# Performance work log

Hardware: AMD Instinct MI355X
Metric: run time of the kernel (lower is better)

Reference implementation:

```python
import jax, jax.numpy as jnp
import numpy as np

NUM_LAYERS = 2      # args.num_layers
EPS = 1e-6          # poincare_to_lorentz eps
NORM_CLIP = 1.0     # exp_map norm_control clip
N, K, F, D = 30000, 32, 256, 128


def _normalize_lorentz(h):
    # project onto hyperboloid: time = sqrt(1 + |space|^2)
    sp = h[:, 1:]
    t = jnp.sqrt(1.0 + jnp.sum(sp * sp, axis=-1, keepdims=True))
    return jnp.concatenate([t, sp], axis=-1)


def _exp_map_zero(v):
    # tangent vector at origin has zero time component (normalize_tan with x=0)
    sp = v[:, 1:]
    ldv = jnp.sum(sp * sp, axis=-1, keepdims=True)          # Lorentz norm^2 of (0, sp)
    nd = jnp.sqrt(jnp.clip(ldv + 1e-9, 1e-10, None))
    t = jnp.minimum(nd, NORM_CLIP)                           # norm_control
    time = jnp.cosh(t)
    space = jnp.sinh(t) * sp / nd
    return _normalize_lorentz(jnp.concatenate([time, space], axis=-1))


def _hyperbolic_mean(nbr, w):
    # nbr: [N, K, D] Lorentz points; w: [N, K] neighbor weights
    k = nbr[..., 1:] / nbr[..., :1]                          # h2k: Klein model
    kn = jnp.clip(jnp.sum(k * k, axis=-1, keepdims=True), 0.0, 0.9)
    lam = w[..., None] / jnp.sqrt(1.0 - kn)                  # weighted Lorentz factors
    k_mean = jnp.sum(lam * k, axis=1) / jnp.sum(lam, axis=1)  # [N, D-1]
    # k2h: Klein -> hyperboloid
    kn2 = jnp.minimum(jnp.sum(k_mean * k_mean, axis=-1, keepdims=True), 0.9)
    ones = jnp.ones((k_mean.shape[0], 1), k_mean.dtype)
    return jnp.concatenate([ones, k_mean], axis=-1) / jnp.sqrt(1.0 - kn2)


def _lorentz_activation(h):
    # lorentz -> poincare, SELU, poincare -> lorentz (c = 1)
    p = h[:, 1:] / (h[:, :1] + 1.0)
    p = jax.nn.selu(p)
    pn = jnp.sum(p * p, axis=-1, keepdims=True)
    return jnp.concatenate([1.0 + pn, 2.0 * p], axis=-1) / (1.0 - pn + EPS)


def setup_inputs() -> dict:
    key = jax.random.key(0)
    k1, k2, k3, k4, k5 = jax.random.split(key, 5)
    x = jax.random.normal(k1, (N, F), dtype=jnp.float32)
    adj = jax.random.randint(k2, (N, K), 0, N, dtype=jnp.int32)
    w = jax.random.uniform(k3, (N, K), dtype=jnp.float32)
    lin_W = jax.random.normal(k4, (F, D), dtype=jnp.float32) / np.sqrt(F)
    lin_b = jnp.zeros((D,), dtype=jnp.float32)
    M, _ = jnp.linalg.qr(jax.random.normal(k5, (D - 1, D - 1), dtype=jnp.float32))  # orthogonal init
    return {"x": x, "adj": adj, "w": w, "lin_W": lin_W, "lin_b": lin_b, "M": M}


def reference(x, adj, w, lin_W, lin_b, M):
    h = jax.nn.selu(x @ lin_W + lin_b)          # Euclidean projection + activation
    h = _exp_map_zero(h)                        # lift to hyperboloid
    d = h.shape[-1]
    # retrieve_params: block-diag [[1,0],[0,M]] Lorentz rotation (tie_weight -> shared)
    lw = jnp.zeros((d, d), h.dtype).at[0, 0].set(1.0).at[1:, 1:].set(M)
    for _ in range(NUM_LAYERS):
        msg = h @ lw                             # Stiefel transform
        nbr = msg[adj]                           # [N, K, D] neighbor gather
        h = _hyperbolic_mean(nbr, w)             # Klein weighted mean
        h = _lorentz_activation(h)               # SELU in Poincare model
        h = _normalize_lorentz(h)                # re-project onto hyperboloid
    return h
```

## Files before the change

### kernel.cpp

```cpp
#include <hip/hip_runtime.h>
#include <hip/hip_fp16.h>
#include <math.h>

#define NN 30000
#define KK 32
#define FF 256
#define DD 128
#define NB16 1875
#define SA 268

typedef _Float16 f16x8 __attribute__((ext_vector_type(8)));
typedef float f32x4v __attribute__((ext_vector_type(4)));

__device__ __forceinline__ float seluf(float x) {
    const float scale = 1.0507009873554804934193349852946f;
    const float alpha = 1.6732632423543772848170429916717f;
    return x > 0.f ? scale * x : scale * alpha * expm1f(x);
}

__device__ __forceinline__ float waveReduceSum(float v) {
#pragma unroll
    for (int m = 1; m < 64; m <<= 1) v += __shfl_xor(v, m, 64);
    return v;
}

__global__ __launch_bounds__(256) void k_prep(
    const float* __restrict__ W, const float* __restrict__ M,
    _Float16* __restrict__ Wt, _Float16* __restrict__ Lt)
{
    const int b = blockIdx.x, t = threadIdx.x;
    if (b < 128) {
        Wt[b * FF + t] = (_Float16)W[t * DD + b];
    } else if (t < 128) {
        const int c = b - 128, k = t;
        const float v = (k == 0 && c == 0) ? 1.f
                      : ((k >= 1 && c >= 1) ? M[(k - 1) * 127 + (c - 1)] : 0.f);
        Lt[c * DD + k] = (_Float16)v;
    }
}

__global__ __launch_bounds__(256) void k_lin_exp_msg(
    const float* __restrict__ x, const _Float16* __restrict__ Wt,
    const float* __restrict__ b, const _Float16* __restrict__ Lt,
    __half* __restrict__ table)
{
    __shared__ _Float16 as_[16][SA];
    __shared__ _Float16 hhi[16][SA];
    __shared__ _Float16 hlo[16][SA];
    __shared__ float red[4][16];
    __shared__ float m0s[16];
    const int wv_ = threadIdx.x >> 6;
    const int lane = threadIdx.x & 63;
    const int g = lane >> 4, c16 = lane & 15;
    const int baseRow = blockIdx.x * 16;
    const int nb = wv_ * 2;
    const int arow = baseRow + c16;

    {
        const float4* xp = (const float4*)(x + (size_t)arow * FF);
#pragma unroll
        for (int i = 0; i < 2; ++i) {
            const int ks = wv_ * 2 + i;
            const float4 f0 = xp[ks * 8 + g * 2];
            const float4 f1 = xp[ks * 8 + g * 2 + 1];
            const float q[8] = {f0.x, f0.y, f0.z, f0.w, f1.x, f1.y, f1.z, f1.w};
            f16x8 a;
#pragma unroll
            for (int j = 0; j < 8; ++j) a[j] = (_Float16)q[j];
            *(f16x8*)&as_[c16][ks * 32 + g * 8] = a;
        }
    }
    __syncthreads();

    f16x8 bw0[8], bw1[8];
#pragma unroll
    for (int ks = 0; ks < 8; ++ks) {
        bw0[ks] = *(const f16x8*)(Wt + (size_t)((nb + 0) * 16 + c16) * FF + ks * 32 + g * 8);
        bw1[ks] = *(const f16x8*)(Wt + (size_t)((nb + 1) * 16 + c16) * FF + ks * 32 + g * 8);
    }
    f16x8 af[8];
#pragma unroll
    for (int ks = 0; ks < 8; ++ks)
        af[ks] = *(const f16x8*)&as_[c16][ks * 32 + g * 8];

    f32x4v acc[2];
    acc[0] = acc[1] = f32x4v{0.f, 0.f, 0.f, 0.f};
#pragma unroll
    for (int ks = 0; ks < 8; ++ks) {
        acc[0] = __builtin_amdgcn_mfma_f32_16x16x32_f16(af[ks], bw0[ks], acc[0], 0, 0, 0);
        acc[1] = __builtin_amdgcn_mfma_f32_16x16x32_f16(af[ks], bw1[ks], acc[1], 0, 0, 0);
    }

    float bias[2];
#pragma unroll
    for (int n = 0; n < 2; ++n) bias[n] = b[(nb + n) * 16 + c16];

    float vv[4][2];
#pragma unroll
    for (int r = 0; r < 4; ++r) {
        float part = 0.f;
#pragma unroll
        for (int n = 0; n < 2; ++n) {
            vv[r][n] = seluf(acc[n][r] + bias[n]);
            float sq = vv[r][n] * vv[r][n];
            if (wv_ == 0 && n == 0 && c16 == 0) sq = 0.f;
            part += sq;
        }
#pragma unroll
        for (int m = 1; m < 16; m <<= 1) part += __shfl_xor(part, m, 64);
        if (c16 == 0) red[wv_][4 * g + r] = part;
    }
    __syncthreads();
#pragma unroll
    for (int r = 0; r < 4; ++r) {
        const int lrow = 4 * g + r;
        const float ldv = red[0][lrow] + red[1][lrow] + red[2][lrow] + red[3][lrow];
        const float nd = sqrtf(fmaxf(ldv + 1e-9f, 1e-10f));
        const float t  = fminf(nd, 1.0f);
        const float sc = sinhf(t) / nd;
        const float tm = sqrtf(1.f + sc * sc * ldv);
#pragma unroll
        for (int n = 0; n < 2; ++n) {
            const int col = (nb + n) * 16 + c16;
            const float o = (wv_ == 0 && n == 0 && c16 == 0) ? tm : sc * vv[r][n];
            const _Float16 hi = (_Float16)o;
            hhi[lrow][col] = hi;
            hlo[lrow][col] = (_Float16)(o - (float)hi);
        }
    }
    __syncthreads();

    f16x8 bl0[4], bl1[4];
#pragma unroll
    for (int ks = 0; ks < 4; ++ks) {
        bl0[ks] = *(const f16x8*)(Lt + (size_t)((nb + 0) * 16 + c16) * DD + ks * 32 + g * 8);
        bl1[ks] = *(const f16x8*)(Lt + (size_t)((nb + 1) * 16 + c16) * DD + ks * 32 + g * 8);
    }
    f16x8 mh[4], ml[4];
#pragma unroll
    for (int ks = 0; ks < 4; ++ks) {
        mh[ks] = *(const f16x8*)&hhi[c16][ks * 32 + g * 8];
        ml[ks] = *(const f16x8*)&hlo[c16][ks * 32 + g * 8];
    }
    acc[0] = acc[1] = f32x4v{0.f, 0.f, 0.f, 0.f};
#pragma unroll
    for (int ks = 0; ks < 4; ++ks) {
        acc[0] = __builtin_amdgcn_mfma_f32_16x16x32_f16(mh[ks], bl0[ks], acc[0], 0, 0, 0);
        acc[0] = __builtin_amdgcn_mfma_f32_16x16x32_f16(ml[ks], bl0[ks], acc[0], 0, 0, 0);
        acc[1] = __builtin_amdgcn_mfma_f32_16x16x32_f16(mh[ks], bl1[ks], acc[1], 0, 0, 0);
        acc[1] = __builtin_amdgcn_mfma_f32_16x16x32_f16(ml[ks], bl1[ks], acc[1], 0, 0, 0);
    }

#pragma unroll
    for (int r = 0; r < 4; ++r) {
        float part = 0.f;
#pragma unroll
        for (int n = 0; n < 2; ++n) {
            float sq = acc[n][r] * acc[n][r];
            if (wv_ == 0 && n == 0 && c16 == 0) sq = 0.f;
            part += sq;
        }
#pragma unroll
        for (int m = 1; m < 16; m <<= 1) part += __shfl_xor(part, m, 64);
        if (c16 == 0) red[wv_][4 * g + r] = part;
        if (wv_ == 0 && c16 == 0) m0s[4 * g + r] = acc[0][r];
    }
    __syncthreads();
#pragma unroll
    for (int r = 0; r < 4; ++r) {
        const int lrow = 4 * g + r;
        const int row = baseRow + lrow;
        const float rn = 1.f / m0s[lrow];
        const float sum2 = red[0][lrow] + red[1][lrow] + red[2][lrow] + red[3][lrow];
        float kn = sum2 * rn * rn;
        kn = fminf(fmaxf(kn, 0.f), 0.9f);
        const float fh = 1.f / sqrtf(1.f - kn);
#pragma unroll
        for (int n = 0; n < 2; ++n) {
            const float val = (wv_ == 0 && n == 0 && c16 == 0) ? fh : acc[n][r] * rn;
            table[(size_t)row * DD + (nb + n) * 16 + c16] = __float2half(val);
        }
    }
}

__global__ __launch_bounds__(256) void k_msg_aux(
    const float* __restrict__ h, const _Float16* __restrict__ Lt,
    __half* __restrict__ table)
{
    __shared__ _Float16 hhi[16][SA];
    __shared__ _Float16 hlo[16][SA];
    __shared__ float red[4][16];
    __shared__ float m0s[16];
    const int wv_ = threadIdx.x >> 6;
    const int lane = threadIdx.x & 63;
    const int g = lane >> 4, c16 = lane & 15;
    const int baseRow = blockIdx.x * 16;
    const int nb = wv_ * 2;
    const int arow = baseRow + c16;

    {
        const float4* hp = (const float4*)(h + (size_t)arow * DD);
        const int ks = wv_;
        const float4 f0 = hp[ks * 8 + g * 2];
        const float4 f1 = hp[ks * 8 + g * 2 + 1];
        const float q[8] = {f0.x, f0.y, f0.z, f0.w, f1.x, f1.y, f1.z, f1.w};
        f16x8 hi, lo;
#pragma unroll
        for (int j = 0; j < 8; ++j) {
            hi[j] = (_Float16)q[j];
            lo[j] = (_Float16)(q[j] - (float)hi[j]);
        }
        *(f16x8*)&hhi[c16][ks * 32 + g * 8] = hi;
        *(f16x8*)&hlo[c16][ks * 32 + g * 8] = lo;
    }
    __syncthreads();

    f16x8 bl0[4], bl1[4];
#pragma unroll
    for (int ks = 0; ks < 4; ++ks) {
        bl0[ks] = *(const f16x8*)(Lt + (size_t)((nb + 0) * 16 + c16) * DD + ks * 32 + g * 8);
        bl1[ks] = *(const f16x8*)(Lt + (size_t)((nb + 1) * 16 + c16) * DD + ks * 32 + g * 8);
    }
    f16x8 mh[4], ml[4];
#pragma unroll
    for (int ks = 0; ks < 4; ++ks) {
        mh[ks] = *(const f16x8*)&hhi[c16][ks * 32 + g * 8];
        ml[ks] = *(const f16x8*)&hlo[c16][ks * 32 + g * 8];
    }
    f32x4v acc[2];
    acc[0] = acc[1] = f32x4v{0.f, 0.f, 0.f, 0.f};
#pragma unroll
    for (int ks = 0; ks < 4; ++ks) {
        acc[0] = __builtin_amdgcn_mfma_f32_16x16x32_f16(mh[ks], bl0[ks], acc[0], 0, 0, 0);
        acc[0] = __builtin_amdgcn_mfma_f32_16x16x32_f16(ml[ks], bl0[ks], acc[0], 0, 0, 0);
        acc[1] = __builtin_amdgcn_mfma_f32_16x16x32_f16(mh[ks], bl1[ks], acc[1], 0, 0, 0);
        acc[1] = __builtin_amdgcn_mfma_f32_16x16x32_f16(ml[ks], bl1[ks], acc[1], 0, 0, 0);
    }

#pragma unroll
    for (int r = 0; r < 4; ++r) {
        float part = 0.f;
#pragma unroll
        for (int n = 0; n < 2; ++n) {
            float sq = acc[n][r] * acc[n][r];
            if (wv_ == 0 && n == 0 && c16 == 0) sq = 0.f;
            part += sq;
        }
#pragma unroll
        for (int m = 1; m < 16; m <<= 1) part += __shfl_xor(part, m, 64);
        if (c16 == 0) red[wv_][4 * g + r] = part;
        if (wv_ == 0 && c16 == 0) m0s[4 * g + r] = acc[0][r];
    }
    __syncthreads();
#pragma unroll
    for (int r = 0; r < 4; ++r) {
        const int lrow = 4 * g + r;
        const int row = baseRow + lrow;
        const float rn = 1.f / m0s[lrow];
        const float sum2 = red[0][lrow] + red[1][lrow] + red[2][lrow] + red[3][lrow];
        float kn = sum2 * rn * rn;
        kn = fminf(fmaxf(kn, 0.f), 0.9f);
        const float fh = 1.f / sqrtf(1.f - kn);
#pragma unroll
        for (int n = 0; n < 2; ++n) {
            const float val = (wv_ == 0 && n == 0 && c16 == 0) ? fh : acc[n][r] * rn;
            table[(size_t)row * DD + (nb + n) * 16 + c16] = __float2half(val);
        }
    }
}

__global__ __launch_bounds__(256) void k_layer(
    const __half* __restrict__ table, const int* __restrict__ adj,
    const float* __restrict__ w, float* __restrict__ out)
{
    const int wave = threadIdx.x >> 6;
    const int lane = threadIdx.x & 63;
    const int node = blockIdx.x * 4 + wave;

    const int   av = adj[node * KK + (lane & 31)];
    const float wv = w[node * KK + (lane & 31)];

    unsigned int vbits[32];
#pragma unroll
    for (int j = 0; j < KK; ++j) {
        const int idx = __shfl(av, j, 64);
        vbits[j] = *(const unsigned int*)(table + (size_t)idx * DD + lane * 2);
    }

    const float f  = __half2float(table[(size_t)av * DD]);
    const float lam = wv * f;
    float ls = lam;
#pragma unroll
    for (int m = 1; m < 32; m <<= 1) ls += __shfl_xor(ls, m, 64);

    float km0 = 0.f, km1 = 0.f;
#pragma unroll
    for (int j = 0; j < KK; ++j) {
        const float cj = __shfl(lam, j, 64);
        const __half2 hh = *(const __half2*)&vbits[j];
        const float2 v = __half22float2(hh);
        km0 = fmaf(cj, v.x, km0);
        km1 = fmaf(cj, v.y, km1);
    }
    const float rl = 1.f / ls;
    const float m0 = km0 * rl;
    const float m1 = km1 * rl;
    float c2 = (lane ? m0 * m0 : 0.f) + m1 * m1;
    const float kn2 = fminf(waveReduceSum(c2), 0.9f);
    const float invs = 1.f / sqrtf(1.f - kn2);
    const float pd = invs + 1.f;
    const float p0 = lane ? seluf(m0 * invs / pd) : 0.f;
    const float p1 = seluf(m1 * invs / pd);
    float pc = p0 * p0 + p1 * p1;
    const float pn = waveReduceSum(pc);
    const float rdn = 1.f / (1.f - pn + 1e-6f);
    const float tm = sqrtf(1.f + 4.f * pn * rdn * rdn);
    float2 o;
    o.x = lane ? 2.f * p0 * rdn : tm;
    o.y = 2.f * p1 * rdn;
    *(float2*)(out + (size_t)node * DD + lane * 2) = o;
}

extern "C" void kernel_launch(void* const* d_in, const int* in_sizes, int n_in,
                              void* d_out, int out_size, void* d_ws, size_t ws_size,
                              hipStream_t stream) {
    const float* x     = (const float*)d_in[0];
    const int*   adj   = (const int*)d_in[1];
    const float* w     = (const float*)d_in[2];
    const float* lin_W = (const float*)d_in[3];
    const float* lin_b = (const float*)d_in[4];
    const float* M     = (const float*)d_in[5];
    float*  h     = (float*)d_out;
    char*   ws    = (char*)d_ws;
    __half*   table = (__half*)ws;
    _Float16* Wt    = (_Float16*)(ws + 7680000);
    _Float16* Lt    = (_Float16*)(ws + 7745536);

    k_prep<<<256, 256, 0, stream>>>(lin_W, M, Wt, Lt);
    k_lin_exp_msg<<<NB16, 256, 0, stream>>>(x, Wt, lin_b, Lt, table);
    k_layer<<<NN / 4, 256, 0, stream>>>(table, adj, w, h);
    k_msg_aux<<<NB16, 256, 0, stream>>>(h, Lt, table);
    k_layer<<<NN / 4, 256, 0, stream>>>(table, adj, w, h);
}
```

Before: 119.5 us.

## Fuse first layer aggregation with second-layer message transform via shared memory

The first layer's gather and aggregate is merged with the following Stiefel message transform into one kernel. Each block aggregates 16 nodes (4 per wave) and writes the hi/lo fp16 split of the result straight into shared memory for the MFMA transform, so the intermediate fp32 h never goes to global memory. This adds a second table buffer and drops one launch. In exchange, each wave now runs four serial gathers before the transform, with fewer blocks than the old per-node layer kernel, which may expose more gather latency.

```diff
diff --git a/kernel.cpp b/kernel.cpp
--- a/kernel.cpp
+++ b/kernel.cpp
@@ -10,6 +10,7 @@
 #define SA 268
 
 typedef _Float16 f16x8 __attribute__((ext_vector_type(8)));
+typedef _Float16 f16x2 __attribute__((ext_vector_type(2)));
 typedef float f32x4v __attribute__((ext_vector_type(4)));
 
 __device__ __forceinline__ float seluf(float x) {
@@ -183,9 +184,10 @@
     }
 }
 
-__global__ __launch_bounds__(256) void k_msg_aux(
-    const float* __restrict__ h, const _Float16* __restrict__ Lt,
-    __half* __restrict__ table)
+__global__ __launch_bounds__(256) void k_layer_msg(
+    const __half* __restrict__ tin, const int* __restrict__ adj,
+    const float* __restrict__ w, const _Float16* __restrict__ Lt,
+    __half* __restrict__ tout)
 {
     __shared__ _Float16 hhi[16][SA];
     __shared__ _Float16 hlo[16][SA];
@@ -194,27 +196,63 @@
     const int wv_ = threadIdx.x >> 6;
     const int lane = threadIdx.x & 63;
     const int g = lane >> 4, c16 = lane & 15;
-    const int baseRow = blockIdx.x * 16;
+    const int baseNode = blockIdx.x * 16;
+
+#pragma unroll
+    for (int q = 0; q < 4; ++q) {
+        const int node = baseNode + wv_ * 4 + q;
+        const int   av = adj[node * KK + (lane & 31)];
+        const float wvv = w[node * KK + (lane & 31)];
+
+        unsigned int vbits[32];
+#pragma unroll
+        for (int j = 0; j < KK; ++j) {
+            const int idx = __shfl(av, j, 64);
+            vbits[j] = *(const unsigned int*)(tin + (size_t)idx * DD + lane * 2);
+        }
+        const float f = __half2float(tin[(size_t)av * DD]);
+        const float lam = wvv * f;
+        float ls = lam;
+#pragma unroll
+        for (int m = 1; m < 32; m <<= 1) ls += __shfl_xor(ls, m, 64);
+
+        float km0 = 0.f, km1 = 0.f;
+#pragma unroll
+        for (int j = 0; j < KK; ++j) {
+            const float cj = __shfl(lam, j, 64);
+            const __half2 hh = *(const __half2*)&vbits[j];
+            const float2 v = __half22float2(hh);
+            km0 = fmaf(cj, v.x, km0);
+            km1 = fmaf(cj, v.y, km1);
+        }
+        const float rl = 1.f / ls;
+        const float m0 = km0 * rl;
+        const float m1 = km1 * rl;
+        float c2 = (lane ? m0 * m0 : 0.f) + m1 * m1;
+        const float kn2 = fminf(waveReduceSum(c2), 0.9f);
+        const float invs = 1.f / sqrtf(1.f - kn2);
+        const float pd = invs + 1.f;
+        const float p0 = lane ? seluf(m0 * invs / pd) : 0.f;
+        const float p1 = seluf(m1 * invs / pd);
+        float pc = p0 * p0 + p1 * p1;
+        const float pn = waveReduceSum(pc);
+        const float rdn = 1.f / (1.f - pn + 1e-6f);
+        const float tm = sqrtf(1.f + 4.f * pn * rdn * rdn);
+        const float ox = lane ? 2.f * p0 * rdn : tm;
+        const float oy = 2.f * p1 * rdn;
+        const int lrow = wv_ * 4 + q;
+        const _Float16 hx = (_Float16)ox;
+        const _Float16 hy = (_Float16)oy;
+        f16x2 hi2, lo2;
+        hi2[0] = hx; hi2[1] = hy;
+        lo2[0] = (_Float16)(ox - (float)hx);
+        lo2[1] = (_Float16)(oy - (float)hy);
+        *(f16x2*)&hhi[lrow][2 * lane] = hi2;
+        *(f16x2*)&hlo[lrow][2 * lane] = lo2;
+    }
+    __syncthreads();
+
     const int nb = wv_ * 2;
-    const int arow = baseRow + c16;
-
-    {
-        const float4* hp = (const float4*)(h + (size_t)arow * DD);
-        const int ks = wv_;
-        const float4 f0 = hp[ks * 8 + g * 2];
-        const float4 f1 = hp[ks * 8 + g * 2 + 1];
-        const float q[8] = {f0.x, f0.y, f0.z, f0.w, f1.x, f1.y, f1.z, f1.w};
-        f16x8 hi, lo;
-#pragma unroll
-        for (int j = 0; j < 8; ++j) {
-            hi[j] = (_Float16)q[j];
-            lo[j] = (_Float16)(q[j] - (float)hi[j]);
-        }
-        *(f16x8*)&hhi[c16][ks * 32 + g * 8] = hi;
-        *(f16x8*)&hlo[c16][ks * 32 + g * 8] = lo;
-    }
-    __syncthreads();
-
     f16x8 bl0[4], bl1[4];
 #pragma unroll
     for (int ks = 0; ks < 4; ++ks) {
@@ -255,7 +293,7 @@
 #pragma unroll
     for (int r = 0; r < 4; ++r) {
         const int lrow = 4 * g + r;
-        const int row = baseRow + lrow;
+        const int row = baseNode + lrow;
         const float rn = 1.f / m0s[lrow];
         const float sum2 = red[0][lrow] + red[1][lrow] + red[2][lrow] + red[3][lrow];
         float kn = sum2 * rn * rn;
@@ -264,7 +302,7 @@
 #pragma unroll
         for (int n = 0; n < 2; ++n) {
             const float val = (wv_ == 0 && n == 0 && c16 == 0) ? fh : acc[n][r] * rn;
-            table[(size_t)row * DD + (nb + n) * 16 + c16] = __float2half(val);
+            tout[(size_t)row * DD + (nb + n) * 16 + c16] = __float2half(val);
         }
     }
 }
@@ -330,15 +368,15 @@
     const float* lin_W = (const float*)d_in[3];
     const float* lin_b = (const float*)d_in[4];
     const float* M     = (const float*)d_in[5];
-    float*  h     = (float*)d_out;
+    float*  out   = (float*)d_out;
     char*   ws    = (char*)d_ws;
-    __half*   table = (__half*)ws;
-    _Float16* Wt    = (_Float16*)(ws + 7680000);
-    _Float16* Lt    = (_Float16*)(ws + 7745536);
+    __half*   table0 = (__half*)ws;
+    __half*   table1 = (__half*)(ws + 7680000);
+    _Float16* Wt     = (_Float16*)(ws + 15360000);
+    _Float16* Lt     = (_Float16*)(ws + 15425536);
 
     k_prep<<<256, 256, 0, stream>>>(lin_W, M, Wt, Lt);
-    k_lin_exp_msg<<<NB16, 256, 0, stream>>>(x, Wt, lin_b, Lt, table);
-    k_layer<<<NN / 4, 256, 0, stream>>>(table, adj, w, h);
-    k_msg_aux<<<NB16, 256, 0, stream>>>(h, Lt, table);
-    k_layer<<<NN / 4, 256, 0, stream>>>(table, adj, w, h);
-}
+    k_lin_exp_msg<<<NB16, 256, 0, stream>>>(x, Wt, lin_b, Lt, table0);
+    k_layer_msg<<<NB16, 256, 0, stream>>>(table0, adj, w, Lt, table1);
+    k_layer<<<NN / 4, 256, 0, stream>>>(table1, adj, w, out);
+}
```

New measurement: 113.0 us (median of 2 runs). 5.4% less time.
